# Optimization experiments

Hardware: AMD Instinct MI355X
Metric: run time of the kernel (lower is better)

## Reference

```python
import jax, jax.numpy as jnp
import numpy as np

EPS_IN = 1e-4   # added to concatenated inputs before variance (as in original)
EPS_OUT = 1e-6  # added after NaN masking (as in original)


def _mdl_masked(a, b):
    """Diagonal-covariance Mahalanobis distance matrix [B,B], NaN-masked, +eps.

    Original TF code builds diag(var), inverts it with tf.linalg.inv and does two
    dense matmuls; mathematically that is an elementwise divide by the per-feature
    variance followed by diff @ diff^T, which is what we compute here.
    """
    in_co = jnp.concatenate((a, b), axis=0) + EPS_IN          # [2B, D]
    var = jnp.var(in_co, axis=0)                              # [D] per-feature variance
    diff = a - b                                              # [B, D]
    q = jnp.einsum('id,jd->ij', diff / var, diff)             # [B, B] = diff @ inv(diag(var)) @ diff^T
    # sqrt of negative entries is NaN in the original; multiply_no_nan zeroes them.
    neg = q < 0.0
    mdist = jnp.where(neg, 0.0, jnp.sqrt(jnp.where(neg, 1.0, q)))
    return mdist + EPS_OUT


def setup_inputs() -> dict:
    key = jax.random.key(0)
    k1, k2, k3 = jax.random.split(key, 3)
    B, D = 8192, 64
    return {
        'anchor': jax.random.normal(k1, (B, D), dtype=jnp.float32),
        'positive': jax.random.normal(k2, (B, D), dtype=jnp.float32),
        'negative': jax.random.normal(k3, (B, D), dtype=jnp.float32),
    }


def reference(anchor, positive, negative):
    ap = _mdl_masked(anchor, positive)   # [B, B]
    an = _mdl_masked(anchor, negative)   # [B, B]
    ap_dis = jnp.sum(ap, axis=-1)        # [B]
    ap_neg = jnp.sum(an, axis=-1)        # [B]
    return (ap_dis, ap_neg)
```

## Files before the change

kernel.cpp:

```cpp
#include <hip/hip_runtime.h>
#include <hip/hip_bf16.h>


typedef short bf16x8 __attribute__((ext_vector_type(8)));
typedef unsigned short u16x8 __attribute__((ext_vector_type(8)));
typedef float f32x4 __attribute__((ext_vector_type(4)));

#define BROWS 8192
#define DFEAT 64
#define NCO   16384
#define EPS_IN  1e-4f
#define EPS_OUT 1e-6f
#define NPART 64

#define WS_EHL_F  24576
#define EHL_PAIR_USHORTS ((size_t)BROWS * 128)

static __device__ inline unsigned short f2bf_rne(float x) {
  unsigned u = __float_as_uint(x);
  unsigned r = (u + 0x7FFF + ((u >> 16) & 1)) >> 16;
  return (unsigned short)r;
}
static __device__ inline float bf2f(unsigned short s) {
  return __uint_as_float(((unsigned)s) << 16);
}

#define GLOAD(gsrc, ldst)                                                  \
  __builtin_amdgcn_global_load_lds(                                        \
      (const __attribute__((address_space(1))) void*)(gsrc),               \
      (__attribute__((address_space(3))) void*)(ldst), 16, 0, 0)

__global__ __launch_bounds__(256) void stats_kernel(
    const float* __restrict__ a, const float* __restrict__ p,
    const float* __restrict__ n, float* __restrict__ part) {
  __shared__ float acc[384];
  int tid = threadIdx.x;
  int bid = blockIdx.x;
  for (int v = tid; v < 384; v += 256) acc[v] = 0.f;
  __syncthreads();
  const float4* A4 = (const float4*)a;
  const float4* P4 = (const float4*)p;
  const float4* N4 = (const float4*)n;
  size_t base = (size_t)bid * 2048 + tid;
  float s[3][4] = {}, q[3][4] = {};
  #pragma unroll
  for (int k = 0; k < 8; ++k) {
    size_t idx = base + k * 256;
    float4 va = A4[idx], vp = P4[idx], vn = N4[idx];
    float ea[4] = {va.x, va.y, va.z, va.w};
    float ep[4] = {vp.x, vp.y, vp.z, vp.w};
    float en[4] = {vn.x, vn.y, vn.z, vn.w};
    #pragma unroll
    for (int f = 0; f < 4; ++f) {
      float x0 = ea[f] + EPS_IN; s[0][f] += x0; q[0][f] += x0 * x0;
      float x1 = ep[f] + EPS_IN; s[1][f] += x1; q[1][f] += x1 * x1;
      float x2 = en[f] + EPS_IN; s[2][f] += x2; q[2][f] += x2 * x2;
    }
  }
  #pragma unroll
  for (int g = 0; g < 3; ++g)
    #pragma unroll
    for (int f = 0; f < 4; ++f) {
      float vs = s[g][f], vq = q[g][f];
      vs += __shfl_xor(vs, 16); vs += __shfl_xor(vs, 32);
      vq += __shfl_xor(vq, 16); vq += __shfl_xor(vq, 32);
      s[g][f] = vs; q[g][f] = vq;
    }
  int lane = tid & 63;
  if (lane < 16) {
    int d0 = lane * 4;
    #pragma unroll
    for (int g = 0; g < 3; ++g)
      #pragma unroll
      for (int f = 0; f < 4; ++f) {
        atomicAdd(&acc[(2 * g) * 64 + d0 + f], s[g][f]);
        atomicAdd(&acc[(2 * g + 1) * 64 + d0 + f], q[g][f]);
      }
  }
  __syncthreads();
  for (int v = tid; v < 384; v += 256)
    part[(size_t)bid * 384 + v] = acc[v];
}

__global__ __launch_bounds__(256) void prep_kernel(
    const float* __restrict__ a, const float* __restrict__ p,
    const float* __restrict__ n, const float* __restrict__ part,
    unsigned short* __restrict__ EHL, float* __restrict__ out) {
  __shared__ float stats_s[384];
  __shared__ float is_s[64];
  int pair = blockIdx.x >> 8;
  int tb   = blockIdx.x & 255;
  int tid  = threadIdx.x;
  if (tid < 32) out[blockIdx.x * 32 + tid] = 8192.0f * EPS_OUT;
  {
    float s1 = 0.f, s2 = 0.f;
    for (int b = 0; b < NPART; ++b) {
      const float* pb = part + (size_t)b * 384;
      s1 += pb[tid];
      if (tid < 128) s2 += pb[256 + tid];
    }
    stats_s[tid] = s1;
    if (tid < 128) stats_s[256 + tid] = s2;
  }
  __syncthreads();
  if (tid < 64) {
    float sa = stats_s[tid], qa = stats_s[64 + tid];
    float sb = pair ? stats_s[256 + tid] : stats_s[128 + tid];
    float qb = pair ? stats_s[320 + tid] : stats_s[192 + tid];
    const float invN = 1.0f / (float)NCO;
    float m = (sa + sb) * invN;
    float v = (qa + qb) * invN - m * m;
    is_s[tid] = 1.0f / sqrtf(v);
  }
  __syncthreads();
  const float* bptr = pair ? n : p;
  unsigned short* dst = EHL + (size_t)pair * EHL_PAIR_USHORTS;
  int c0 = tid & 7;
  int rl = tid >> 3;
  int row = tb * 32 + rl;
  int d0 = c0 * 8;
  const float* ar = a    + (size_t)row * DFEAT + d0;
  const float* br = bptr + (size_t)row * DFEAT + d0;
  float4 a0 = *(const float4*)(ar);
  float4 a1 = *(const float4*)(ar + 4);
  float4 b0 = *(const float4*)(br);
  float4 b1 = *(const float4*)(br + 4);
  float e[8] = {a0.x - b0.x, a0.y - b0.y, a0.z - b0.z, a0.w - b0.w,
                a1.x - b1.x, a1.y - b1.y, a1.z - b1.z, a1.w - b1.w};
  u16x8 vh, vl;
  #pragma unroll
  for (int j = 0; j < 8; ++j) {
    float ej = e[j] * is_s[d0 + j];
    unsigned short hi = f2bf_rne(ej);
    vh[j] = hi;
    vl[j] = f2bf_rne(ej - bf2f(hi));
  }
  int cs = c0 ^ (row & 7);
  char* drow = (char*)dst + (size_t)row * 256;
  *(u16x8*)(drow + cs * 16)       = vh;
  *(u16x8*)(drow + (8 + cs) * 16) = vl;
}

__global__ __launch_bounds__(256, 2) void mdist_mfma(
    const unsigned short* __restrict__ EHL, float* __restrict__ out) {
  __shared__ __align__(16) unsigned char smem[32768];
  unsigned char* sB0 = smem;
  unsigned char* sB1 = smem + 16384;
  int bid = blockIdx.x;
  int sw  = (bid & 7) * 128 + (bid >> 3);
  int pair = sw >> 9;
  int ib   = (sw >> 3) & 63;
  int r0   = sw & 7;
  const char* base = (const char*)(EHL + (size_t)pair * EHL_PAIR_USHORTS);
  const char* gA = base + (size_t)ib * 32768;
  int tid = threadIdx.x;
  int smax = (ib < 32) ? 32 : 31;
  int nT   = ((smax - r0) / 8 + 1) * 2;

  #pragma unroll
  for (int rr = 0; rr < 8; ++rr) {
    int off = rr * 4096 + tid * 16;
    GLOAD(gA + off, smem + off);
  }
  __syncthreads();

  int lane = tid & 63, w = tid >> 6;
  int wr = w >> 1, wc = w & 1;
  int l15 = lane & 15, lg = lane >> 4;

  bf16x8 af[4][4];
  #pragma unroll
  for (int hk = 0; hk < 4; ++hk) {
    int c = ((hk >> 1) << 3) | ((hk & 1) << 2) | lg;
    #pragma unroll
    for (int m = 0; m < 4; ++m) {
      int rr = wr * 64 + m * 16 + l15;
      int cs = c ^ (rr & 7);
      af[hk][m] = *(const bf16x8*)(smem + rr * 256 + cs * 16);
    }
  }
  __syncthreads();

  {
    const char* gB0 = base + (size_t)((ib + r0) & 63) * 32768;
    #pragma unroll
    for (int rr = 0; rr < 4; ++rr) {
      int off = rr * 4096 + tid * 16;
      GLOAD(gB0 + off, sB0 + off);
    }
  }
  __syncthreads();

  float rs[4][4];
  #pragma unroll
  for (int m = 0; m < 4; ++m)
    #pragma unroll
    for (int rr = 0; rr < 4; ++rr) rs[m][rr] = 0.f;

  const f32x4 zacc = {0.f, 0.f, 0.f, 0.f};
  const int AH[3] = {0, 0, 1};
  const int BH[3] = {0, 1, 0};

  for (int t = 0; t < nT; ++t) {
    unsigned char* wbuf = (t & 1) ? sB0 : sB1;
    const unsigned char* rbuf = (t & 1) ? sB1 : sB0;
    int s   = r0 + 8 * (t >> 1);
    int sub = t & 1;
    if (t + 1 < nT) {
      int tn = t + 1;
      int sn = r0 + 8 * (tn >> 1);
      const char* gs = base + (size_t)((ib + sn) & 63) * 32768 + (tn & 1) * 16384;
      #pragma unroll
      for (int rr = 0; rr < 4; ++rr) {
        int off = rr * 4096 + tid * 16;
        GLOAD(gs + off, wbuf + off);
      }
    }
    bf16x8 bf[4][2];
    #pragma unroll
    for (int hk = 0; hk < 4; ++hk) {
      int c = ((hk >> 1) << 3) | ((hk & 1) << 2) | lg;
      #pragma unroll
      for (int nn = 0; nn < 2; ++nn) {
        int rr = wc * 32 + nn * 16 + l15;
        int cs = c ^ (rr & 7);
        bf[hk][nn] = *(const bf16x8*)(rbuf + rr * 256 + cs * 16);
      }
    }
    f32x4 acc[4][2];
    #pragma unroll
    for (int tt = 0; tt < 3; ++tt) {
      #pragma unroll
      for (int ks = 0; ks < 2; ++ks) {
        int ahk = (AH[tt] << 1) | ks;
        int bhk = (BH[tt] << 1) | ks;
        #pragma unroll
        for (int m = 0; m < 4; ++m) {
          #pragma unroll
          for (int nn = 0; nn < 2; ++nn)
            acc[m][nn] = __builtin_amdgcn_mfma_f32_16x16x32_bf16(
                af[ahk][m], bf[bhk][nn],
                (tt == 0 && ks == 0) ? zacc : acc[m][nn], 0, 0, 0);
        }
      }
    }
    if (s == 0) {
      #pragma unroll
      for (int m = 0; m < 4; ++m)
        #pragma unroll
        for (int nn = 0; nn < 2; ++nn)
          #pragma unroll
          for (int rr = 0; rr < 4; ++rr)
            rs[m][rr] += __builtin_amdgcn_sqrtf(fmaxf(acc[m][nn][rr], 0.f));
    } else {
      float cq0 = 0.f, cq1 = 0.f;
      #pragma unroll
      for (int m = 0; m < 4; ++m)
        #pragma unroll
        for (int nn = 0; nn < 2; ++nn)
          #pragma unroll
          for (int rr = 0; rr < 4; ++rr) {
            float f = __builtin_amdgcn_sqrtf(fmaxf(acc[m][nn][rr], 0.f));
            rs[m][rr] += f;
            if (nn == 0) cq0 += f; else cq1 += f;
          }
      cq0 += __shfl_xor(cq0, 16); cq0 += __shfl_xor(cq0, 32);
      cq1 += __shfl_xor(cq1, 16); cq1 += __shfl_xor(cq1, 32);
      if (lane < 16) {
        int jb = (ib + s) & 63;
        float* orow = &out[pair * BROWS + jb * 128 + sub * 64 + wc * 32 + l15];
        atomicAdd(orow, cq0);
        atomicAdd(orow + 16, cq1);
      }
    }
    __syncthreads();
  }

  #pragma unroll
  for (int m = 0; m < 4; ++m)
    #pragma unroll
    for (int rr = 0; rr < 4; ++rr) {
      float v = rs[m][rr];
      v += __shfl_xor(v, 1);
      v += __shfl_xor(v, 2);
      v += __shfl_xor(v, 4);
      v += __shfl_xor(v, 8);
      rs[m][rr] = v;
    }
  if (l15 == 0) {
    int i0 = ib * 128 + wr * 64;
    #pragma unroll
    for (int m = 0; m < 4; ++m)
      #pragma unroll
      for (int rr = 0; rr < 4; ++rr)
        atomicAdd(&out[pair * BROWS + i0 + m * 16 + lg * 4 + rr], rs[m][rr]);
  }
}

extern "C" void kernel_launch(void* const* d_in, const int* in_sizes, int n_in,
                              void* d_out, int out_size, void* d_ws, size_t ws_size,
                              hipStream_t stream) {
  const float* anchor   = (const float*)d_in[0];
  const float* positive = (const float*)d_in[1];
  const float* negative = (const float*)d_in[2];
  float* out = (float*)d_out;
  float* ws  = (float*)d_ws;

  float* part = ws;
  unsigned short* EHL = (unsigned short*)(ws + WS_EHL_F);

  stats_kernel<<<64, 256, 0, stream>>>(anchor, positive, negative, part);
  prep_kernel<<<512, 256, 0, stream>>>(anchor, positive, negative, part, EHL, out);
  mdist_mfma<<<1024, 256, 0, stream>>>(EHL, out);
}
```

Before: 125.1 us.

## Stage full 128-row B tiles per iteration and widen stats partial reduction

The distance kernel now loads a whole 128-row B block (32 KB) per iteration into two 32 KB LDS buffers and processes both 64-column halves from it. This halves the number of barriers and load issues per output tile, and the grid drops from 1024 to 512 blocks with each block covering more column blocks. The stats kernel is spread over 256 blocks instead of 64 to improve parallelism, which gives prep_kernel four times as many partials to sum. The larger LDS footprint (64 KB per block) may limit occupancy, and the smaller grid may underfill the GPU.

```diff
diff --git a/kernel.cpp b/kernel.cpp
--- a/kernel.cpp
+++ b/kernel.cpp
@@ -11,9 +11,9 @@
 #define NCO   16384
 #define EPS_IN  1e-4f
 #define EPS_OUT 1e-6f
-#define NPART 64
-
-#define WS_EHL_F  24576
+#define NPART 256
+
+#define WS_EHL_F  98560
 #define EHL_PAIR_USHORTS ((size_t)BROWS * 128)
 
 static __device__ inline unsigned short f2bf_rne(float x) {
@@ -41,10 +41,10 @@
   const float4* A4 = (const float4*)a;
   const float4* P4 = (const float4*)p;
   const float4* N4 = (const float4*)n;
-  size_t base = (size_t)bid * 2048 + tid;
+  size_t base = (size_t)bid * 512 + tid;
   float s[3][4] = {}, q[3][4] = {};
   #pragma unroll
-  for (int k = 0; k < 8; ++k) {
+  for (int k = 0; k < 2; ++k) {
     size_t idx = base + k * 256;
     float4 va = A4[idx], vp = P4[idx], vn = N4[idx];
     float ea[4] = {va.x, va.y, va.z, va.w};
@@ -94,6 +94,7 @@
   if (tid < 32) out[blockIdx.x * 32 + tid] = 8192.0f * EPS_OUT;
   {
     float s1 = 0.f, s2 = 0.f;
+    #pragma unroll 8
     for (int b = 0; b < NPART; ++b) {
       const float* pb = part + (size_t)b * 384;
       s1 += pb[tid];
@@ -143,24 +144,25 @@
 
 __global__ __launch_bounds__(256, 2) void mdist_mfma(
     const unsigned short* __restrict__ EHL, float* __restrict__ out) {
-  __shared__ __align__(16) unsigned char smem[32768];
-  unsigned char* sB0 = smem;
-  unsigned char* sB1 = smem + 16384;
+  __shared__ __align__(16) unsigned char buf0[32768];
+  __shared__ __align__(16) unsigned char buf1[32768];
   int bid = blockIdx.x;
-  int sw  = (bid & 7) * 128 + (bid >> 3);
-  int pair = sw >> 9;
-  int ib   = (sw >> 3) & 63;
-  int r0   = sw & 7;
+  int sw  = (bid & 7) * 64 + (bid >> 3);
+  int pair  = sw >> 8;
+  int ib    = (sw >> 2) & 63;
+  int half  = (sw >> 1) & 1;
+  int squad = sw & 1;
   const char* base = (const char*)(EHL + (size_t)pair * EHL_PAIR_USHORTS);
   const char* gA = base + (size_t)ib * 32768;
   int tid = threadIdx.x;
+  int s0   = half + 2 * squad;
   int smax = (ib < 32) ? 32 : 31;
-  int nT   = ((smax - r0) / 8 + 1) * 2;
+  int nOut = (smax - s0) / 4 + 1;
 
   #pragma unroll
   for (int rr = 0; rr < 8; ++rr) {
     int off = rr * 4096 + tid * 16;
-    GLOAD(gA + off, smem + off);
+    GLOAD(gA + off, buf0 + off);
   }
   __syncthreads();
 
@@ -176,20 +178,19 @@
     for (int m = 0; m < 4; ++m) {
       int rr = wr * 64 + m * 16 + l15;
       int cs = c ^ (rr & 7);
-      af[hk][m] = *(const bf16x8*)(smem + rr * 256 + cs * 16);
+      af[hk][m] = *(const bf16x8*)(buf0 + rr * 256 + cs * 16);
     }
   }
   __syncthreads();
 
   {
-    const char* gB0 = base + (size_t)((ib + r0) & 63) * 32768;
-    #pragma unroll
-    for (int rr = 0; rr < 4; ++rr) {
+    const char* gB0 = base + (size_t)((ib + s0) & 63) * 32768;
+    #pragma unroll
+    for (int rr = 0; rr < 8; ++rr) {
       int off = rr * 4096 + tid * 16;
-      GLOAD(gB0 + off, sB0 + off);
-    }
-  }
-  __syncthreads();
+      GLOAD(gB0 + off, buf0 + off);
+    }
+  }
 
   float rs[4][4];
   #pragma unroll
@@ -201,79 +202,80 @@
   const int AH[3] = {0, 0, 1};
   const int BH[3] = {0, 1, 0};
 
-  for (int t = 0; t < nT; ++t) {
-    unsigned char* wbuf = (t & 1) ? sB0 : sB1;
-    const unsigned char* rbuf = (t & 1) ? sB1 : sB0;
-    int s   = r0 + 8 * (t >> 1);
-    int sub = t & 1;
-    if (t + 1 < nT) {
-      int tn = t + 1;
-      int sn = r0 + 8 * (tn >> 1);
-      const char* gs = base + (size_t)((ib + sn) & 63) * 32768 + (tn & 1) * 16384;
-      #pragma unroll
-      for (int rr = 0; rr < 4; ++rr) {
+  for (int t = 0; t < nOut; ++t) {
+    __syncthreads();
+    const unsigned char* rbuf = (t & 1) ? buf1 : buf0;
+    unsigned char* wbuf = (t & 1) ? buf0 : buf1;
+    int s = s0 + 4 * t;
+    if (t + 1 < nOut) {
+      int sn = s0 + 4 * (t + 1);
+      const char* gs = base + (size_t)((ib + sn) & 63) * 32768;
+      #pragma unroll
+      for (int rr = 0; rr < 8; ++rr) {
         int off = rr * 4096 + tid * 16;
         GLOAD(gs + off, wbuf + off);
       }
     }
-    bf16x8 bf[4][2];
-    #pragma unroll
-    for (int hk = 0; hk < 4; ++hk) {
-      int c = ((hk >> 1) << 3) | ((hk & 1) << 2) | lg;
-      #pragma unroll
-      for (int nn = 0; nn < 2; ++nn) {
-        int rr = wc * 32 + nn * 16 + l15;
-        int cs = c ^ (rr & 7);
-        bf[hk][nn] = *(const bf16x8*)(rbuf + rr * 256 + cs * 16);
-      }
-    }
-    f32x4 acc[4][2];
-    #pragma unroll
-    for (int tt = 0; tt < 3; ++tt) {
-      #pragma unroll
-      for (int ks = 0; ks < 2; ++ks) {
-        int ahk = (AH[tt] << 1) | ks;
-        int bhk = (BH[tt] << 1) | ks;
+    #pragma unroll
+    for (int sub = 0; sub < 2; ++sub) {
+      bf16x8 bf[4][2];
+      #pragma unroll
+      for (int hk = 0; hk < 4; ++hk) {
+        int c = ((hk >> 1) << 3) | ((hk & 1) << 2) | lg;
         #pragma unroll
-        for (int m = 0; m < 4; ++m) {
+        for (int nn = 0; nn < 2; ++nn) {
+          int rr = sub * 64 + wc * 32 + nn * 16 + l15;
+          int cs = c ^ (rr & 7);
+          bf[hk][nn] = *(const bf16x8*)(rbuf + rr * 256 + cs * 16);
+        }
+      }
+      f32x4 acc[4][2];
+      #pragma unroll
+      for (int tt = 0; tt < 3; ++tt) {
+        #pragma unroll
+        for (int ks = 0; ks < 2; ++ks) {
+          int ahk = (AH[tt] << 1) | ks;
+          int bhk = (BH[tt] << 1) | ks;
+          #pragma unroll
+          for (int m = 0; m < 4; ++m) {
+            #pragma unroll
+            for (int nn = 0; nn < 2; ++nn)
+              acc[m][nn] = __builtin_amdgcn_mfma_f32_16x16x32_bf16(
+                  af[ahk][m], bf[bhk][nn],
+                  (tt == 0 && ks == 0) ? zacc : acc[m][nn], 0, 0, 0);
+          }
+        }
+      }
+      if (s == 0) {
+        #pragma unroll
+        for (int m = 0; m < 4; ++m)
           #pragma unroll
           for (int nn = 0; nn < 2; ++nn)
-            acc[m][nn] = __builtin_amdgcn_mfma_f32_16x16x32_bf16(
-                af[ahk][m], bf[bhk][nn],
-                (tt == 0 && ks == 0) ? zacc : acc[m][nn], 0, 0, 0);
+            #pragma unroll
+            for (int rr = 0; rr < 4; ++rr)
+              rs[m][rr] += __builtin_amdgcn_sqrtf(fmaxf(acc[m][nn][rr], 0.f));
+      } else {
+        float cq0 = 0.f, cq1 = 0.f;
+        #pragma unroll
+        for (int m = 0; m < 4; ++m)
+          #pragma unroll
+          for (int nn = 0; nn < 2; ++nn)
+            #pragma unroll
+            for (int rr = 0; rr < 4; ++rr) {
+              float f = __builtin_amdgcn_sqrtf(fmaxf(acc[m][nn][rr], 0.f));
+              rs[m][rr] += f;
+              if (nn == 0) cq0 += f; else cq1 += f;
+            }
+        cq0 += __shfl_xor(cq0, 16); cq0 += __shfl_xor(cq0, 32);
+        cq1 += __shfl_xor(cq1, 16); cq1 += __shfl_xor(cq1, 32);
+        if (lane < 16) {
+          int jb = (ib + s) & 63;
+          float* orow = &out[pair * BROWS + jb * 128 + sub * 64 + wc * 32 + l15];
+          atomicAdd(orow, cq0);
+          atomicAdd(orow + 16, cq1);
         }
       }
     }
-    if (s == 0) {
-      #pragma unroll
-      for (int m = 0; m < 4; ++m)
-        #pragma unroll
-        for (int nn = 0; nn < 2; ++nn)
-          #pragma unroll
-          for (int rr = 0; rr < 4; ++rr)
-            rs[m][rr] += __builtin_amdgcn_sqrtf(fmaxf(acc[m][nn][rr], 0.f));
-    } else {
-      float cq0 = 0.f, cq1 = 0.f;
-      #pragma unroll
-      for (int m = 0; m < 4; ++m)
-        #pragma unroll
-        for (int nn = 0; nn < 2; ++nn)
-          #pragma unroll
-          for (int rr = 0; rr < 4; ++rr) {
-            float f = __builtin_amdgcn_sqrtf(fmaxf(acc[m][nn][rr], 0.f));
-            rs[m][rr] += f;
-            if (nn == 0) cq0 += f; else cq1 += f;
-          }
-      cq0 += __shfl_xor(cq0, 16); cq0 += __shfl_xor(cq0, 32);
-      cq1 += __shfl_xor(cq1, 16); cq1 += __shfl_xor(cq1, 32);
-      if (lane < 16) {
-        int jb = (ib + s) & 63;
-        float* orow = &out[pair * BROWS + jb * 128 + sub * 64 + wc * 32 + l15];
-        atomicAdd(orow, cq0);
-        atomicAdd(orow + 16, cq1);
-      }
-    }
-    __syncthreads();
   }
 
   #pragma unroll
@@ -309,7 +311,7 @@
   float* part = ws;
   unsigned short* EHL = (unsigned short*)(ws + WS_EHL_F);
 
-  stats_kernel<<<64, 256, 0, stream>>>(anchor, positive, negative, part);
+  stats_kernel<<<256, 256, 0, stream>>>(anchor, positive, negative, part);
   prep_kernel<<<512, 256, 0, stream>>>(anchor, positive, negative, part, EHL, out);
-  mdist_mfma<<<1024, 256, 0, stream>>>(EHL, out);
-}
+  mdist_mfma<<<512, 256, 0, stream>>>(EHL, out);
+}
```

Result: slower. 167.7 us (+34.1%).
